# Kernel tuning notes

Hardware: AMD Instinct MI355X
Metric: run time of the kernel (lower is better)

## Reference

```python
import jax, jax.numpy as jnp
import numpy as np

B, T, H = 32, 512, 1024

def setup_inputs() -> dict:
    key = jax.random.key(0)
    k1, k2, k3, k4, k5 = jax.random.split(key, 5)
    s = 1.0 / np.sqrt(H)  # torch LSTM init scale
    return {
        "x": jax.random.normal(k1, (B, T, H), dtype=jnp.float32),
        "w_ih": jax.random.uniform(k2, (4 * H, H), jnp.float32, -s, s),
        "w_hh": jax.random.uniform(k3, (4 * H, H), jnp.float32, -s, s),
        "b_ih": jax.random.uniform(k4, (4 * H,), jnp.float32, -s, s),
        "b_hh": jax.random.uniform(k5, (4 * H,), jnp.float32, -s, s),
    }

def reference(x, w_ih, w_hh, b_ih, b_hh):
    # Precompute input projections for all steps: [T, B, 4H]
    xg = jnp.einsum('bth,gh->tbg', x, w_ih) + b_ih + b_hh
    h0 = jnp.zeros((x.shape[0], H), x.dtype)
    c0 = jnp.zeros_like(h0)

    def step(carry, xg_t):
        h, c = carry
        gates = xg_t + h @ w_hh.T            # [B, 4H]
        i, f, g, o = jnp.split(gates, 4, axis=-1)  # torch order: i,f,g,o
        i = jax.nn.sigmoid(i)
        f = jax.nn.sigmoid(f)
        g = jnp.tanh(g)
        o = jax.nn.sigmoid(o)
        c = f * c + i * g
        h = o * jnp.tanh(c)
        return (h, c), None

    (h_n, _), _ = jax.lax.scan(step, (h0, c0), xg)
    return h_n  # [B, H] == h_n[0] in torch
```

## Files before the change

### kernel.cpp

```cpp
#include <hip/hip_runtime.h>
#include <cmath>

#define Tn 512
#define Bn 32
#define Hn 1024

typedef short bf16x8 __attribute__((ext_vector_type(8)));
typedef float f32x4 __attribute__((ext_vector_type(4)));

__device__ __forceinline__ unsigned short f2bf_rne(float f) {
    unsigned u = __float_as_uint(f);
    unsigned r = (u + 0x7fffu + ((u >> 16) & 1u)) >> 16;
    return (unsigned short)r;
}
__device__ __forceinline__ float bf2f(unsigned short h) {
    return __uint_as_float((unsigned)h << 16);
}
__device__ __forceinline__ bf16x8 cvt8(float4 a, float4 b) {
    union { unsigned u[4]; bf16x8 v; } o;
    o.u[0] = (unsigned)f2bf_rne(a.x) | ((unsigned)f2bf_rne(a.y) << 16);
    o.u[1] = (unsigned)f2bf_rne(a.z) | ((unsigned)f2bf_rne(a.w) << 16);
    o.u[2] = (unsigned)f2bf_rne(b.x) | ((unsigned)f2bf_rne(b.y) << 16);
    o.u[3] = (unsigned)f2bf_rne(b.z) | ((unsigned)f2bf_rne(b.w) << 16);
    return o.v;
}
__device__ __forceinline__ bf16x8 as_bf8(uint4 u) {
    union { uint4 q; bf16x8 v; } o; o.q = u; return o.v;
}

__device__ __forceinline__ float fsigf(float x) {
    return __builtin_amdgcn_rcpf(1.f + __expf(-x));
}
__device__ __forceinline__ float ftanhf(float x) {
    return 1.f - 2.f * __builtin_amdgcn_rcpf(1.f + __expf(2.f * x));
}

__device__ __forceinline__ void gstore_u32_nd(unsigned* p, unsigned v) {
    asm volatile("global_store_dword %0, %1, off sc0 sc1"
                 :: "v"(p), "v"(v) : "memory");
}
__device__ __forceinline__ unsigned gload_u32_sc(const unsigned* p) {
    unsigned r;
    asm volatile("global_load_dword %0, %1, off sc0 sc1\n\t"
                 "s_waitcnt vmcnt(0)"
                 : "=&v"(r) : "v"(p) : "memory");
    return r;
}
__device__ __forceinline__ void gload_h_sc(const unsigned short* b0,
                                           const unsigned short* b1,
                                           uint4* o0, uint4* o1) {
    asm volatile(
        "global_load_dwordx4 %0, %8, off sc0 sc1\n\t"
        "global_load_dwordx4 %1, %8, off offset:64 sc0 sc1\n\t"
        "global_load_dwordx4 %2, %8, off offset:128 sc0 sc1\n\t"
        "global_load_dwordx4 %3, %8, off offset:192 sc0 sc1\n\t"
        "global_load_dwordx4 %4, %9, off sc0 sc1\n\t"
        "global_load_dwordx4 %5, %9, off offset:64 sc0 sc1\n\t"
        "global_load_dwordx4 %6, %9, off offset:128 sc0 sc1\n\t"
        "global_load_dwordx4 %7, %9, off offset:192 sc0 sc1\n\t"
        "s_waitcnt vmcnt(0)"
        : "=&v"(o0[0]), "=&v"(o0[1]), "=&v"(o0[2]), "=&v"(o0[3]),
          "=&v"(o1[0]), "=&v"(o1[1]), "=&v"(o1[2]), "=&v"(o1[3])
        : "v"(b0), "v"(b1)
        : "memory");
}

__global__ void lstm_flags_init(unsigned* cnt) { cnt[threadIdx.x] = 0u; }

__global__ __launch_bounds__(512, 2) void lstm_persist_mfma(
    const float* __restrict__ x,
    const float* __restrict__ w_ih,
    const float* __restrict__ w_hh,
    const float* __restrict__ b_ih,
    const float* __restrict__ b_hh,
    unsigned short* __restrict__ hbuf,
    unsigned* __restrict__ cnt,
    float* __restrict__ out)
{
    extern __shared__ char smem[];
    unsigned short* lds_w = (unsigned short*)smem;
    float* lds_r = (float*)(smem + 131584);
    unsigned* lds_cnt = (unsigned*)(smem + 131584 + 18432);

    const int tid = threadIdx.x;
    const int bj  = blockIdx.x;
    const int wv  = tid >> 6;
    const int ln  = tid & 63;
    const int l15 = ln & 15;
    const int qd  = ln >> 4;

    if (tid == 0) *lds_cnt = 0u;

    for (int i = 0; i < 16; ++i) {
        int slot = i * 512 + tid;
        int r    = slot >> 9;
        int f4   = slot & 511;
        int n    = (r >> 2) * Hn + bj * 4 + (r & 3);
        float4 v = (f4 < 256) ? ((const float4*)(w_ih + (size_t)n * Hn))[f4]
                              : ((const float4*)(w_hh + (size_t)n * Hn))[f4 - 256];
        unsigned short h0 = f2bf_rne(v.x), h1 = f2bf_rne(v.y);
        unsigned short h2 = f2bf_rne(v.z), h3 = f2bf_rne(v.w);
        unsigned short l0 = f2bf_rne(v.x - bf2f(h0)), l1 = f2bf_rne(v.y - bf2f(h1));
        unsigned short l2 = f2bf_rne(v.z - bf2f(h2)), l3 = f2bf_rne(v.w - bf2f(h3));
        uint2 ph, pl;
        ph.x = (unsigned)h0 | ((unsigned)h1 << 16);
        ph.y = (unsigned)h2 | ((unsigned)h3 << 16);
        pl.x = (unsigned)l0 | ((unsigned)l1 << 16);
        pl.y = (unsigned)l2 | ((unsigned)l3 << 16);
        *(uint2*)(lds_w + (size_t)r        * 2056 + f4 * 4) = ph;
        *(uint2*)(lds_w + (size_t)(r + 16) * 2056 + f4 * 4) = pl;
    }

    float bias0 = 0.f, bias1 = 0.f, bias2 = 0.f, bias3 = 0.f, creg = 0.f;
    int fb = 0, fcl = 0;
    if (ln < 16) {
        const int e = (wv << 4) | ln;
        fb  = e >> 2;
        fcl = e & 3;
        int col = bj * 4 + fcl;
        bias0 = b_ih[col]          + b_hh[col];
        bias1 = b_ih[Hn + col]     + b_hh[Hn + col];
        bias2 = b_ih[2 * Hn + col] + b_hh[2 * Hn + col];
        bias3 = b_ih[3 * Hn + col] + b_hh[3 * Hn + col];
    }
    __syncthreads();

    const unsigned short* whi_base = lds_w + (size_t)l15 * 2056 + qd * 8;
    const unsigned short* wlo_base = lds_w + (size_t)(l15 + 16) * 2056 + qd * 8;
    const float* xr0 = x + (size_t)l15        * (Tn * Hn) + wv * 128 + qd * 8;
    const float* xr1 = x + (size_t)(16 + l15) * (Tn * Hn) + wv * 128 + qd * 8;
    const size_t hoff0 = (size_t)l15        * Hn + wv * 128 + qd * 8;
    const size_t hoff1 = (size_t)(16 + l15) * Hn + wv * 128 + qd * 8;

    float4 xa0[4], xb0[4], xa1[4], xb1[4];
    #pragma unroll
    for (int j = 0; j < 4; ++j) {
        xa0[j] = *(const float4*)(xr0 + j * 32);
        xb0[j] = *(const float4*)(xr0 + j * 32 + 4);
        xa1[j] = *(const float4*)(xr1 + j * 32);
        xb1[j] = *(const float4*)(xr1 + j * 32 + 4);
    }

    for (int t = 0; t < Tn; ++t) {
        f32x4 a0h = {0.f,0.f,0.f,0.f}, a0l = {0.f,0.f,0.f,0.f};
        f32x4 a1h = {0.f,0.f,0.f,0.f}, a1l = {0.f,0.f,0.f,0.f};

        float4 na0[4], nb0[4], na1[4], nb1[4];
        {
            const int tn = (t + 1 < Tn) ? (t + 1) : t;
            const float* p0 = xr0 + (size_t)tn * Hn;
            const float* p1 = xr1 + (size_t)tn * Hn;
            #pragma unroll
            for (int j = 0; j < 4; ++j) {
                na0[j] = *(const float4*)(p0 + j * 32);
                nb0[j] = *(const float4*)(p0 + j * 32 + 4);
                na1[j] = *(const float4*)(p1 + j * 32);
                nb1[j] = *(const float4*)(p1 + j * 32 + 4);
            }
        }

        #pragma unroll
        for (int j = 0; j < 4; ++j) {
            const int koff = wv * 128 + j * 32;
            bf16x8 ahi = *(const bf16x8*)(whi_base + koff);
            bf16x8 alo = *(const bf16x8*)(wlo_base + koff);
            bf16x8 bf0 = cvt8(xa0[j], xb0[j]);
            bf16x8 bf1 = cvt8(xa1[j], xb1[j]);
            a0h = __builtin_amdgcn_mfma_f32_16x16x32_bf16(ahi, bf0, a0h, 0, 0, 0);
            a0l = __builtin_amdgcn_mfma_f32_16x16x32_bf16(alo, bf0, a0l, 0, 0, 0);
            a1h = __builtin_amdgcn_mfma_f32_16x16x32_bf16(ahi, bf1, a1h, 0, 0, 0);
            a1l = __builtin_amdgcn_mfma_f32_16x16x32_bf16(alo, bf1, a1l, 0, 0, 0);
        }

        if (t > 0) {
            if (wv == 0) {
                const unsigned thr = 256u * (((unsigned)(t - 1) >> 3) + 1u);
                const unsigned* cp = cnt + ((t - 1) & 7) * 16;
                while (gload_u32_sc(cp) < thr)
                    __builtin_amdgcn_s_sleep(1);
            }
            __syncthreads();

            const unsigned short* hb = hbuf + (size_t)((t - 1) & 1) * (Bn * Hn);
            uint4 hf0[4], hf1[4];
            gload_h_sc(hb + hoff0, hb + hoff1, hf0, hf1);
            #pragma unroll
            for (int j = 0; j < 4; ++j) {
                const int koff = 1024 + wv * 128 + j * 32;
                bf16x8 ahi = *(const bf16x8*)(whi_base + koff);
                bf16x8 alo = *(const bf16x8*)(wlo_base + koff);
                bf16x8 bf0 = as_bf8(hf0[j]);
                bf16x8 bf1 = as_bf8(hf1[j]);
                a0h = __builtin_amdgcn_mfma_f32_16x16x32_bf16(ahi, bf0, a0h, 0, 0, 0);
                a0l = __builtin_amdgcn_mfma_f32_16x16x32_bf16(alo, bf0, a0l, 0, 0, 0);
                a1h = __builtin_amdgcn_mfma_f32_16x16x32_bf16(ahi, bf1, a1h, 0, 0, 0);
                a1l = __builtin_amdgcn_mfma_f32_16x16x32_bf16(alo, bf1, a1l, 0, 0, 0);
            }
        }

        {
            f32x4 acc0 = a0h + a0l;
            f32x4 acc1 = a1h + a1l;
            float* pr0 = lds_r + (wv * 2 + 0) * 288 + l15;
            float* pr1 = lds_r + (wv * 2 + 1) * 288 + l15;
            #pragma unroll
            for (int r = 0; r < 4; ++r) {
                pr0[(qd * 4 + r) * 18] = acc0[r];
                pr1[(qd * 4 + r) * 18] = acc1[r];
            }
        }
        __syncthreads();

        if (ln < 16) {
            const int bt = fb >> 4, c16 = fb & 15;
            float s0 = 0.f, s1 = 0.f, s2 = 0.f, s3 = 0.f;
            #pragma unroll
            for (int w8 = 0; w8 < 8; ++w8) {
                const float* base = lds_r + (w8 * 2 + bt) * 288 + c16;
                s0 += base[(0 * 4 + fcl) * 18];
                s1 += base[(1 * 4 + fcl) * 18];
                s2 += base[(2 * 4 + fcl) * 18];
                s3 += base[(3 * 4 + fcl) * 18];
            }
            float iv = fsigf(s0 + bias0);
            float fv = fsigf(s1 + bias1);
            float gv = ftanhf(s2 + bias2);
            float ov = fsigf(s3 + bias3);
            creg = fv * creg + iv * gv;
            float hn = ov * ftanhf(creg);
            unsigned short hv = f2bf_rne(hn);
            unsigned up = (unsigned)__shfl_xor((int)(unsigned)hv, 1, 64);
            if (!(ln & 1)) {
                unsigned pack = (unsigned)hv | (up << 16);
                unsigned short* hw = hbuf + (size_t)(t & 1) * (Bn * Hn)
                                   + (size_t)fb * Hn + bj * 4 + fcl;
                gstore_u32_nd((unsigned*)hw, pack);
            }
            if (t == Tn - 1) out[(size_t)fb * Hn + bj * 4 + fcl] = hn;
        }
        asm volatile("s_waitcnt vmcnt(0)" ::: "memory");
        if (ln == 0) {
            unsigned old = atomicAdd(lds_cnt, 1u);
            if (old == 8u * (unsigned)t + 7u && (t + 1 < Tn))
                atomicAdd(cnt + (t & 7) * 16, 1u);
        }

        #pragma unroll
        for (int j = 0; j < 4; ++j) {
            xa0[j] = na0[j]; xb0[j] = nb0[j];
            xa1[j] = na1[j]; xb1[j] = nb1[j];
        }
    }
}

extern "C" void kernel_launch(void* const* d_in, const int* in_sizes, int n_in,
                              void* d_out, int out_size, void* d_ws, size_t ws_size,
                              hipStream_t stream) {
    const float* x    = (const float*)d_in[0];
    const float* w_ih = (const float*)d_in[1];
    const float* w_hh = (const float*)d_in[2];
    const float* b_ih = (const float*)d_in[3];
    const float* b_hh = (const float*)d_in[4];
    float* out = (float*)d_out;

    char* ws = (char*)d_ws;
    unsigned*       cnt  = (unsigned*)ws;
    unsigned short* hbuf = (unsigned short*)(ws + 1024);
    (void)in_sizes; (void)n_in; (void)out_size; (void)ws_size;

    const size_t smem_bytes = 131584 + 18432 + 16;

    lstm_flags_init<<<dim3(1), dim3(256), 0, stream>>>(cnt);
    lstm_persist_mfma<<<dim3(256), dim3(512), smem_bytes, stream>>>(
        x, w_ih, w_hh, b_ih, b_hh, hbuf, cnt, out);
}
```

Baseline: 4.158 ms.

## Replace global counter barrier with per-block step flags and LDS wave flags

The grid-wide step barrier changes from one shared atomic counter, polled by wave 0, to a per-block flag holding the step number. Every wave polls a slice of the 256 flags itself, which removes the block-level __syncthreads after the poll. The intra-block reduction barrier is also replaced by per-wave LDS step flags that waves spin on. Four extra waves per block spin on dummy FMAs until the compute waves finish, apparently to keep the compute unit busy or its clocks up; they compete for issue slots with the real waves and add power draw.

```diff
diff --git a/kernel.cpp b/kernel.cpp
--- a/kernel.cpp
+++ b/kernel.cpp
@@ -65,22 +65,22 @@
         : "memory");
 }
 
-__global__ void lstm_flags_init(unsigned* cnt) { cnt[threadIdx.x] = 0u; }
-
-__global__ __launch_bounds__(512, 2) void lstm_persist_mfma(
+__global__ void lstm_flags_init(unsigned* flags) { flags[threadIdx.x] = 0u; }
+
+__global__ __launch_bounds__(768, 1) void lstm_persist_mfma(
     const float* __restrict__ x,
     const float* __restrict__ w_ih,
     const float* __restrict__ w_hh,
     const float* __restrict__ b_ih,
     const float* __restrict__ b_hh,
     unsigned short* __restrict__ hbuf,
-    unsigned* __restrict__ cnt,
+    unsigned* __restrict__ flags,
     float* __restrict__ out)
 {
     extern __shared__ char smem[];
     unsigned short* lds_w = (unsigned short*)smem;
     float* lds_r = (float*)(smem + 131584);
-    unsigned* lds_cnt = (unsigned*)(smem + 131584 + 18432);
+    unsigned* lds_u = (unsigned*)(smem + 131584 + 18432);
 
     const int tid = threadIdx.x;
     const int bj  = blockIdx.x;
@@ -89,41 +89,65 @@
     const int l15 = ln & 15;
     const int qd  = ln >> 4;
 
-    if (tid == 0) *lds_cnt = 0u;
-
-    for (int i = 0; i < 16; ++i) {
-        int slot = i * 512 + tid;
-        int r    = slot >> 9;
-        int f4   = slot & 511;
-        int n    = (r >> 2) * Hn + bj * 4 + (r & 3);
-        float4 v = (f4 < 256) ? ((const float4*)(w_ih + (size_t)n * Hn))[f4]
-                              : ((const float4*)(w_hh + (size_t)n * Hn))[f4 - 256];
-        unsigned short h0 = f2bf_rne(v.x), h1 = f2bf_rne(v.y);
-        unsigned short h2 = f2bf_rne(v.z), h3 = f2bf_rne(v.w);
-        unsigned short l0 = f2bf_rne(v.x - bf2f(h0)), l1 = f2bf_rne(v.y - bf2f(h1));
-        unsigned short l2 = f2bf_rne(v.z - bf2f(h2)), l3 = f2bf_rne(v.w - bf2f(h3));
-        uint2 ph, pl;
-        ph.x = (unsigned)h0 | ((unsigned)h1 << 16);
-        ph.y = (unsigned)h2 | ((unsigned)h3 << 16);
-        pl.x = (unsigned)l0 | ((unsigned)l1 << 16);
-        pl.y = (unsigned)l2 | ((unsigned)l3 << 16);
-        *(uint2*)(lds_w + (size_t)r        * 2056 + f4 * 4) = ph;
-        *(uint2*)(lds_w + (size_t)(r + 16) * 2056 + f4 * 4) = pl;
-    }
-
     float bias0 = 0.f, bias1 = 0.f, bias2 = 0.f, bias3 = 0.f, creg = 0.f;
     int fb = 0, fcl = 0;
-    if (ln < 16) {
-        const int e = (wv << 4) | ln;
-        fb  = e >> 2;
-        fcl = e & 3;
-        int col = bj * 4 + fcl;
-        bias0 = b_ih[col]          + b_hh[col];
-        bias1 = b_ih[Hn + col]     + b_hh[Hn + col];
-        bias2 = b_ih[2 * Hn + col] + b_hh[2 * Hn + col];
-        bias3 = b_ih[3 * Hn + col] + b_hh[3 * Hn + col];
+
+    if (wv < 8) {
+        if (tid == 0) {
+            lds_u[0] = 0u;
+            lds_u[1] = 0u;
+            #pragma unroll
+            for (int i = 0; i < 8; ++i) lds_u[2 + i] = 0u;
+        }
+        for (int i = 0; i < 16; ++i) {
+            int slot = i * 512 + tid;
+            int r    = slot >> 9;
+            int f4   = slot & 511;
+            int n    = (r >> 2) * Hn + bj * 4 + (r & 3);
+            float4 v = (f4 < 256) ? ((const float4*)(w_ih + (size_t)n * Hn))[f4]
+                                  : ((const float4*)(w_hh + (size_t)n * Hn))[f4 - 256];
+            unsigned short h0 = f2bf_rne(v.x), h1 = f2bf_rne(v.y);
+            unsigned short h2 = f2bf_rne(v.z), h3 = f2bf_rne(v.w);
+            unsigned short l0 = f2bf_rne(v.x - bf2f(h0)), l1 = f2bf_rne(v.y - bf2f(h1));
+            unsigned short l2 = f2bf_rne(v.z - bf2f(h2)), l3 = f2bf_rne(v.w - bf2f(h3));
+            uint2 ph, pl;
+            ph.x = (unsigned)h0 | ((unsigned)h1 << 16);
+            ph.y = (unsigned)h2 | ((unsigned)h3 << 16);
+            pl.x = (unsigned)l0 | ((unsigned)l1 << 16);
+            pl.y = (unsigned)l2 | ((unsigned)l3 << 16);
+            *(uint2*)(lds_w + (size_t)r        * 2056 + f4 * 4) = ph;
+            *(uint2*)(lds_w + (size_t)(r + 16) * 2056 + f4 * 4) = pl;
+        }
+        if (ln < 16) {
+            const int e = (wv << 4) | ln;
+            fb  = e >> 2;
+            fcl = e & 3;
+            int col = bj * 4 + fcl;
+            bias0 = b_ih[col]          + b_hh[col];
+            bias1 = b_ih[Hn + col]     + b_hh[Hn + col];
+            bias2 = b_ih[2 * Hn + col] + b_hh[2 * Hn + col];
+            bias3 = b_ih[3 * Hn + col] + b_hh[3 * Hn + col];
+        }
     }
+
     __syncthreads();
+
+    if (wv >= 8) {
+        volatile unsigned* dn = lds_u + 1;
+        float z0 = 1.f + (float)tid * 1e-7f;
+        float z1 = z0 * 1.1f, z2 = z0 * 1.2f, z3 = z0 * 1.3f;
+        while (*dn == 0u) {
+            #pragma unroll
+            for (int i = 0; i < 64; ++i) {
+                z0 = __builtin_fmaf(z0, 1.0000001f, 1e-30f);
+                z1 = __builtin_fmaf(z1, 1.0000001f, 1e-30f);
+                z2 = __builtin_fmaf(z2, 1.0000001f, 1e-30f);
+                z3 = __builtin_fmaf(z3, 1.0000001f, 1e-30f);
+            }
+        }
+        asm volatile("" :: "v"(z0), "v"(z1), "v"(z2), "v"(z3));
+        return;
+    }
 
     const unsigned short* whi_base = lds_w + (size_t)l15 * 2056 + qd * 8;
     const unsigned short* wlo_base = lds_w + (size_t)(l15 + 16) * 2056 + qd * 8;
@@ -173,14 +197,15 @@
         }
 
         if (t > 0) {
-            if (wv == 0) {
-                const unsigned thr = 256u * (((unsigned)(t - 1) >> 3) + 1u);
-                const unsigned* cp = cnt + ((t - 1) & 7) * 16;
-                while (gload_u32_sc(cp) < thr)
-                    __builtin_amdgcn_s_sleep(1);
-            }
-            __syncthreads();
-
+            {
+                const int src = (ln < 32) ? (wv * 32 + ln) : bj;
+                const unsigned* fp = flags + src;
+                bool done = false;
+                for (;;) {
+                    if (!done) done = (gload_u32_sc(fp) >= (unsigned)t);
+                    if (__all((int)done)) break;
+                }
+            }
             const unsigned short* hb = hbuf + (size_t)((t - 1) & 1) * (Bn * Hn);
             uint4 hf0[4], hf1[4];
             gload_h_sc(hb + hoff0, hb + hoff1, hf0, hf1);
@@ -209,7 +234,17 @@
                 pr1[(qd * 4 + r) * 18] = acc1[r];
             }
         }
-        __syncthreads();
+        asm volatile("s_waitcnt lgkmcnt(0)" ::: "memory");
+        if (ln == 0) ((volatile unsigned*)(lds_u + 2))[wv] = (unsigned)(t + 1);
+        {
+            bool ok;
+            do {
+                unsigned v = 0xffffffffu;
+                if (ln < 8) v = ((volatile unsigned*)(lds_u + 2))[ln];
+                ok = (v >= (unsigned)(t + 1));
+            } while (!__all((int)ok));
+        }
+        asm volatile("" ::: "memory");
 
         if (ln < 16) {
             const int bt = fb >> 4, c16 = fb & 15;
@@ -240,9 +275,9 @@
         }
         asm volatile("s_waitcnt vmcnt(0)" ::: "memory");
         if (ln == 0) {
-            unsigned old = atomicAdd(lds_cnt, 1u);
+            unsigned old = atomicAdd(&lds_u[0], 1u);
             if (old == 8u * (unsigned)t + 7u && (t + 1 < Tn))
-                atomicAdd(cnt + (t & 7) * 16, 1u);
+                gstore_u32_nd(&flags[bj], (unsigned)(t + 1));
         }
 
         #pragma unroll
@@ -251,6 +286,8 @@
             xa1[j] = na1[j]; xb1[j] = nb1[j];
         }
     }
+
+    if (tid == 0) ((volatile unsigned*)lds_u)[1] = 1u;
 }
 
 extern "C" void kernel_launch(void* const* d_in, const int* in_sizes, int n_in,
@@ -264,13 +301,13 @@
     float* out = (float*)d_out;
 
     char* ws = (char*)d_ws;
-    unsigned*       cnt  = (unsigned*)ws;
-    unsigned short* hbuf = (unsigned short*)(ws + 1024);
+    unsigned*       flags = (unsigned*)ws;
+    unsigned short* hbuf  = (unsigned short*)(ws + 1024);
     (void)in_sizes; (void)n_in; (void)out_size; (void)ws_size;
 
-    const size_t smem_bytes = 131584 + 18432 + 16;
-
-    lstm_flags_init<<<dim3(1), dim3(256), 0, stream>>>(cnt);
-    lstm_persist_mfma<<<dim3(256), dim3(512), smem_bytes, stream>>>(
-        x, w_ih, w_hh, b_ih, b_hh, hbuf, cnt, out);
-}
+    const size_t smem_bytes = 131584 + 18432 + 64;
+
+    lstm_flags_init<<<dim3(1), dim3(256), 0, stream>>>(flags);
+    lstm_persist_mfma<<<dim3(256), dim3(768), smem_bytes, stream>>>(
+        x, w_ih, w_hh, b_ih, b_hh, hbuf, flags, out);
+}
```

Result: faster. 3.929 ms (-5.5%).

## Replace global atomic step counter with per-block flags polled by each wave

Applied to the files above, without the earlier changes.

Each block now publishes its progress by storing the next step index to its own flag instead of atomically incrementing a shared counter. Each wave polls only the 32 producer flags covering its slice of h, using a wave vote, and skips the block-wide __syncthreads. The h history buffer is indexed by the full timestep rather than double-buffered, so h loads become ordinary cached loads with no reuse hazard. The aim is to cut atomic contention and global-barrier latency on the serial recurrence. In exchange the workspace must hold all T steps of h, and correctness now relies on the memory ordering between the flag store and the h data.

```diff
diff --git a/kernel.cpp b/kernel.cpp
--- a/kernel.cpp
+++ b/kernel.cpp
@@ -39,6 +39,11 @@
     asm volatile("global_store_dword %0, %1, off sc0 sc1"
                  :: "v"(p), "v"(v) : "memory");
 }
+__device__ __forceinline__ void gstore_u32_sc(unsigned* p, unsigned v) {
+    asm volatile("global_store_dword %0, %1, off sc0 sc1\n\t"
+                 "s_waitcnt vmcnt(0)"
+                 :: "v"(p), "v"(v) : "memory");
+}
 __device__ __forceinline__ unsigned gload_u32_sc(const unsigned* p) {
     unsigned r;
     asm volatile("global_load_dword %0, %1, off sc0 sc1\n\t"
@@ -46,26 +51,8 @@
                  : "=&v"(r) : "v"(p) : "memory");
     return r;
 }
-__device__ __forceinline__ void gload_h_sc(const unsigned short* b0,
-                                           const unsigned short* b1,
-                                           uint4* o0, uint4* o1) {
-    asm volatile(
-        "global_load_dwordx4 %0, %8, off sc0 sc1\n\t"
-        "global_load_dwordx4 %1, %8, off offset:64 sc0 sc1\n\t"
-        "global_load_dwordx4 %2, %8, off offset:128 sc0 sc1\n\t"
-        "global_load_dwordx4 %3, %8, off offset:192 sc0 sc1\n\t"
-        "global_load_dwordx4 %4, %9, off sc0 sc1\n\t"
-        "global_load_dwordx4 %5, %9, off offset:64 sc0 sc1\n\t"
-        "global_load_dwordx4 %6, %9, off offset:128 sc0 sc1\n\t"
-        "global_load_dwordx4 %7, %9, off offset:192 sc0 sc1\n\t"
-        "s_waitcnt vmcnt(0)"
-        : "=&v"(o0[0]), "=&v"(o0[1]), "=&v"(o0[2]), "=&v"(o0[3]),
-          "=&v"(o1[0]), "=&v"(o1[1]), "=&v"(o1[2]), "=&v"(o1[3])
-        : "v"(b0), "v"(b1)
-        : "memory");
-}
-
-__global__ void lstm_flags_init(unsigned* cnt) { cnt[threadIdx.x] = 0u; }
+
+__global__ void lstm_flags_init(unsigned* flags) { flags[threadIdx.x] = 0u; }
 
 __global__ __launch_bounds__(512, 2) void lstm_persist_mfma(
     const float* __restrict__ x,
@@ -74,7 +61,7 @@
     const float* __restrict__ b_ih,
     const float* __restrict__ b_hh,
     unsigned short* __restrict__ hbuf,
-    unsigned* __restrict__ cnt,
+    unsigned* __restrict__ flags,
     float* __restrict__ out)
 {
     extern __shared__ char smem[];
@@ -173,17 +160,22 @@
         }
 
         if (t > 0) {
-            if (wv == 0) {
-                const unsigned thr = 256u * (((unsigned)(t - 1) >> 3) + 1u);
-                const unsigned* cp = cnt + ((t - 1) & 7) * 16;
-                while (gload_u32_sc(cp) < thr)
-                    __builtin_amdgcn_s_sleep(1);
-            }
-            __syncthreads();
-
-            const unsigned short* hb = hbuf + (size_t)((t - 1) & 1) * (Bn * Hn);
+            {
+                const int src = (ln < 32) ? (wv * 32 + ln) : bj;
+                const unsigned* fp = flags + src;
+                bool done = false;
+                for (;;) {
+                    if (!done) done = (gload_u32_sc(fp) >= (unsigned)t);
+                    if (__all((int)done)) break;
+                }
+            }
+            const unsigned short* hb = hbuf + (size_t)(t - 1) * (Bn * Hn);
             uint4 hf0[4], hf1[4];
-            gload_h_sc(hb + hoff0, hb + hoff1, hf0, hf1);
+            #pragma unroll
+            for (int j = 0; j < 4; ++j) {
+                hf0[j] = *(const uint4*)(hb + hoff0 + j * 32);
+                hf1[j] = *(const uint4*)(hb + hoff1 + j * 32);
+            }
             #pragma unroll
             for (int j = 0; j < 4; ++j) {
                 const int koff = 1024 + wv * 128 + j * 32;
@@ -232,7 +224,7 @@
             unsigned up = (unsigned)__shfl_xor((int)(unsigned)hv, 1, 64);
             if (!(ln & 1)) {
                 unsigned pack = (unsigned)hv | (up << 16);
-                unsigned short* hw = hbuf + (size_t)(t & 1) * (Bn * Hn)
+                unsigned short* hw = hbuf + (size_t)t * (Bn * Hn)
                                    + (size_t)fb * Hn + bj * 4 + fcl;
                 gstore_u32_nd((unsigned*)hw, pack);
             }
@@ -242,7 +234,7 @@
         if (ln == 0) {
             unsigned old = atomicAdd(lds_cnt, 1u);
             if (old == 8u * (unsigned)t + 7u && (t + 1 < Tn))
-                atomicAdd(cnt + (t & 7) * 16, 1u);
+                gstore_u32_sc(&flags[bj], (unsigned)(t + 1));
         }
 
         #pragma unroll
@@ -264,13 +256,13 @@
     float* out = (float*)d_out;
 
     char* ws = (char*)d_ws;
-    unsigned*       cnt  = (unsigned*)ws;
-    unsigned short* hbuf = (unsigned short*)(ws + 1024);
+    unsigned*       flags = (unsigned*)ws;
+    unsigned short* hbuf  = (unsigned short*)(ws + 1024);
     (void)in_sizes; (void)n_in; (void)out_size; (void)ws_size;
 
     const size_t smem_bytes = 131584 + 18432 + 16;
 
-    lstm_flags_init<<<dim3(1), dim3(256), 0, stream>>>(cnt);
+    lstm_flags_init<<<dim3(1), dim3(256), 0, stream>>>(flags);
     lstm_persist_mfma<<<dim3(256), dim3(512), smem_bytes, stream>>>(
-        x, w_ih, w_hh, b_ih, b_hh, hbuf, cnt, out);
-}
+        x, w_ih, w_hh, b_ih, b_hh, hbuf, flags, out);
+}
```

Result: faster. 4.009 ms (-3.6%).
